# Kernel optimization log

Measured on AMD Instinct MI355X. Metric: run time of the kernel, lower is better.

Reference implementation:

```python
import jax, jax.numpy as jnp
import numpy as np

B, S, D, H = 2, 2048, 2048, 16
HD = D // H


def setup_inputs() -> dict:
    key = jax.random.key(0)
    kx, = jax.random.split(key, 1)
    return {
        "x": jax.random.normal(kx, (B, S, D), dtype=jnp.float32),
        "q_mask": jnp.ones((D, D), dtype=jnp.float32),
        "k_mask": jnp.ones((D, D), dtype=jnp.float32),
        "v_mask": jnp.ones((D, D), dtype=jnp.float32),
        "out_mask": jnp.ones((D, D), dtype=jnp.float32),
        "head_mask": jnp.ones((H,), dtype=jnp.float32),
        "attention_mask": jnp.ones((B, S), dtype=jnp.float32),
        "shared_weight": jnp.float32(1.0),
    }


def reference(x, q_mask, k_mask, v_mask, out_mask, head_mask, attention_mask, shared_weight):
    b, s, d = x.shape
    scale = jnp.float32(HD) ** -0.5

    def shared_linear(inp, mask):
        # F.linear(x, mask * shared_weight): out = inp @ (mask*sw).T
        return jnp.einsum("bsd,ed->bse", inp, mask * shared_weight)

    q = shared_linear(x, q_mask).reshape(b, s, H, HD).transpose(0, 2, 1, 3)  # [B,H,S,HD]
    k = shared_linear(x, k_mask).reshape(b, s, H, HD).transpose(0, 2, 1, 3)
    v = shared_linear(x, v_mask).reshape(b, s, H, HD).transpose(0, 2, 1, 3)

    hm = head_mask.reshape(1, H, 1, 1)
    q, k, v = q * hm, k * hm, v * hm

    scores = jnp.einsum("bhqd,bhkd->bhqk", q, k) * scale  # [B,H,S,S]

    # causal mask: upper triangle (j > i) -> -inf
    causal = jnp.triu(jnp.ones((s, s), dtype=bool), k=1)
    scores = jnp.where(causal, -jnp.inf, scores)

    # additive attention mask: (1 - m) * -10000, broadcast [B,1,1,S]
    scores = scores + (1.0 - attention_mask)[:, None, None, :] * -10000.0

    attn = jax.nn.softmax(scores, axis=-1)  # dropout is identity in eval / p=0

    out = jnp.einsum("bhqk,bhkd->bhqd", attn, v)          # [B,H,S,HD]
    out = out.transpose(0, 2, 1, 3).reshape(b, s, d)       # [B,S,D]
    return shared_linear(out, out_mask)
```

## Files before the change

kernel.cpp:

```cpp
#include <hip/hip_runtime.h>

#define B_  2
#define S_  2048
#define D_  2048
#define H_  16
#define HD_ 128

typedef __bf16 bf16;
typedef __bf16 bf16x4 __attribute__((ext_vector_type(4)));
typedef __bf16 bf16x8 __attribute__((ext_vector_type(8)));
typedef float  f32x4  __attribute__((ext_vector_type(4)));

__device__ __forceinline__ void gld_lds16(const void* g, void* l) {
    __builtin_amdgcn_global_load_lds(
        (const __attribute__((address_space(1))) unsigned int*)g,
        (__attribute__((address_space(3))) unsigned int*)l, 16, 0, 0);
}

__global__ __launch_bounds__(256)
void precast_kernel(const float* __restrict__ x, bf16* __restrict__ xh,
                    bf16* __restrict__ xl) {
    int i = (blockIdx.x * 256 + threadIdx.x) * 8;
    float4 a = *(const float4*)(x + i);
    float4 b = *(const float4*)(x + i + 4);
    float av[8] = {a.x, a.y, a.z, a.w, b.x, b.y, b.z, b.w};
    bf16x8 h8, l8;
#pragma unroll
    for (int e = 0; e < 8; e++) {
        bf16 hv = (bf16)av[e];
        h8[e] = hv;
        l8[e] = (bf16)(av[e] - (float)hv);
    }
    *(bf16x8*)(xh + i) = h8;
    *(bf16x8*)(xl + i) = l8;
}

__global__ __launch_bounds__(256)
void transpose_v(const bf16* __restrict__ vp, bf16* __restrict__ vt) {
    const int bh = blockIdx.x >> 5;
    const int s0 = (blockIdx.x & 31) * 64;
    const int t = threadIdx.x;
    __shared__ bf16 tile[128 * 72];
    const bf16* src = vp + (size_t)bh * S_ * HD_;
    bf16* dst = vt + (size_t)bh * HD_ * S_;

    {
        int r = t >> 2;
        int g = (t & 3) * 4;
#pragma unroll
        for (int w = 0; w < 4; w++) {
            bf16x8 v8 = *(const bf16x8*)&src[(size_t)(s0 + r) * HD_ + (g + w) * 8];
#pragma unroll
            for (int e = 0; e < 8; e++) tile[((g + w) * 8 + e) * 72 + r] = v8[e];
        }
    }
    __syncthreads();
    {
        int d = t >> 1;
        int sg0 = (t & 1) * 4;
#pragma unroll
        for (int w = 0; w < 4; w++) {
            int sg = sg0 + w;
            *(bf16x8*)&dst[(size_t)d * S_ + s0 + sg * 8] =
                *(const bf16x8*)&tile[d * 72 + sg * 8];
        }
    }
}

#define BK 64

template<int MODE>
__global__ __launch_bounds__(256, 3)
void gemm_nt(const bf16* __restrict__ Ah_g, const bf16* __restrict__ Al_g,
             const float* __restrict__ B0, const float* __restrict__ B1,
             const float* __restrict__ B2,
             const float* __restrict__ swp, const float* __restrict__ hm,
             bf16* __restrict__ qh_, bf16* __restrict__ ql_,
             bf16* __restrict__ kh_, bf16* __restrict__ kl_,
             bf16* __restrict__ vp_, float* __restrict__ Cf) {
    const int K = D_;
    __shared__ bf16 Ah[128 * 64];
    __shared__ bf16 Al[128 * 64];
    __shared__ bf16 Bs[128 * 64];
    const int t = threadIdx.x;
    const int wave = t >> 6, lane = t & 63;
    const int wr = wave >> 1, wc = wave & 1;
    const int m0 = blockIdx.y * 128, n0 = blockIdx.x * 128;
    const int lrow = lane & 15, lquad = lane >> 4;
    const float sw = swp[0];

    const int which = (MODE == 0) ? (n0 >> 11) : 0;
    const bool split = (MODE == 0) && (which < 2);

    const float* Bp;
    if (MODE == 0) {
        Bp = (which == 0) ? B0 : ((which == 1) ? B1 : B2);
        Bp += (size_t)(n0 & (D_ - 1)) * K;
    } else {
        Bp = B0 + (size_t)n0 * K;
    }

    const int srow8 = lane >> 3;
    const int sgrp  = lane & 7;
    const int g0 = (lquad)     ^ (lrow & 7);
    const int g1 = (lquad + 4) ^ (lrow & 7);

    f32x4 acc[4][4];
#pragma unroll
    for (int i = 0; i < 4; i++)
#pragma unroll
        for (int j = 0; j < 4; j++) acc[i][j] = (f32x4){0.f, 0.f, 0.f, 0.f};

    for (int k0 = 0; k0 < K; k0 += BK) {
#pragma unroll
        for (int p = 0; p < 4; p++) {
            int r = wave * 32 + p * 8 + srow8;
            int gcol = (sgrp ^ (r & 7)) * 8;
            gld_lds16(Ah_g + (size_t)(m0 + r) * K + k0 + gcol,
                      &Ah[(wave * 32 + p * 8) * 64]);
            if (split)
                gld_lds16(Al_g + (size_t)(m0 + r) * K + k0 + gcol,
                          &Al[(wave * 32 + p * 8) * 64]);
        }
#pragma unroll
        for (int p = 0; p < 4; p++) {
            int r = p * 32 + (t >> 3);
            int gcol = (sgrp ^ (r & 7)) * 8;
            const float* bp = Bp + (size_t)r * K + k0 + gcol;
            float4 blo = *(const float4*)bp;
            float4 bhi = *(const float4*)(bp + 4);
            bf16x8 b8;
            b8[0] = (bf16)(blo.x * sw); b8[1] = (bf16)(blo.y * sw);
            b8[2] = (bf16)(blo.z * sw); b8[3] = (bf16)(blo.w * sw);
            b8[4] = (bf16)(bhi.x * sw); b8[5] = (bf16)(bhi.y * sw);
            b8[6] = (bf16)(bhi.z * sw); b8[7] = (bf16)(bhi.w * sw);
            *(bf16x8*)&Bs[r * 64 + sgrp * 8] = b8;
        }
        __syncthreads();

#pragma unroll
        for (int kk = 0; kk < 2; kk++) {
            const int gA = kk ? g1 : g0;
            bf16x8 afh[4], afl[4], bfr[4];
#pragma unroll
            for (int i = 0; i < 4; i++) {
                int row = wr * 64 + i * 16 + lrow;
                afh[i] = *(const bf16x8*)&Ah[row * 64 + gA * 8];
                if (split) afl[i] = *(const bf16x8*)&Al[row * 64 + gA * 8];
            }
#pragma unroll
            for (int j = 0; j < 4; j++) {
                int row = wc * 64 + j * 16 + lrow;
                bfr[j] = *(const bf16x8*)&Bs[row * 64 + gA * 8];
            }
#pragma unroll
            for (int i = 0; i < 4; i++)
#pragma unroll
                for (int j = 0; j < 4; j++) {
                    acc[i][j] = __builtin_amdgcn_mfma_f32_16x16x32_bf16(
                        afh[i], bfr[j], acc[i][j], 0, 0, 0);
                    if (split)
                        acc[i][j] = __builtin_amdgcn_mfma_f32_16x16x32_bf16(
                            afl[i], bfr[j], acc[i][j], 0, 0, 0);
                }
        }
        __syncthreads();
    }

#pragma unroll
    for (int i = 0; i < 4; i++) {
#pragma unroll
        for (int j = 0; j < 4; j++) {
#pragma unroll
            for (int r = 0; r < 4; r++) {
                int m = m0 + wr * 64 + i * 16 + lquad * 4 + r;
                int n = n0 + wc * 64 + j * 16 + lrow;
                float v = acc[i][j][r];
                if (MODE == 0) {
                    int e = n & (D_ - 1);
                    int h = e >> 7, hd = e & (HD_ - 1);
                    int b = m >> 11, s = m & (S_ - 1);
                    v *= hm[h];
                    size_t idx = (((size_t)b * H_ + h) * S_ + s) * HD_ + hd;
                    if (which == 2) {
                        vp_[idx] = (bf16)v;
                    } else {
                        bf16 hv = (bf16)v;
                        bf16 lv = (bf16)(v - (float)hv);
                        if (which == 0) { qh_[idx] = hv; ql_[idx] = lv; }
                        else            { kh_[idx] = hv; kl_[idx] = lv; }
                    }
                } else {
                    Cf[(size_t)m * D_ + n] = v;
                }
            }
        }
    }
}

#define SPLD 72

__global__ __launch_bounds__(256, 2)
void attn_kernel(const bf16* __restrict__ qh_, const bf16* __restrict__ ql_,
                 const bf16* __restrict__ kh_, const bf16* __restrict__ kl_,
                 const bf16* __restrict__ vt_, const float* __restrict__ am,
                 bf16* __restrict__ outp) {
    const int bh = blockIdx.x & 31;
    const int qblk = 31 - (blockIdx.x >> 5);
    const int b = bh >> 4, h = bh & 15;
    const int i0 = qblk * 64;
    const int t = threadIdx.x, wave = t >> 6, lane = t & 63;
    const int lrow = lane & 15, quad = lane >> 4;

    __shared__ bf16 skh[64 * 128];
    __shared__ bf16 skl[64 * 128];
    __shared__ bf16 svt[128 * 64];
    __shared__ bf16 sp[4][16 * SPLD];

    const size_t kbase = (size_t)bh * S_ * HD_;
    const size_t vbase = (size_t)bh * HD_ * S_;

    const int qrow = i0 + wave * 16 + lrow;
    bf16x8 qhf[4], qlf[4];
#pragma unroll
    for (int c = 0; c < 4; c++) {
        qhf[c] = *(const bf16x8*)&qh_[kbase + (size_t)qrow * HD_ + c * 32 + quad * 8];
        qlf[c] = *(const bf16x8*)&ql_[kbase + (size_t)qrow * HD_ + c * 32 + quad * 8];
    }

    float m_i[4], l_i[4];
    f32x4 O[8];
#pragma unroll
    for (int r = 0; r < 4; r++) { m_i[r] = -INFINITY; l_i[r] = 0.f; }
#pragma unroll
    for (int n2 = 0; n2 < 8; n2++) O[n2] = (f32x4){0.f, 0.f, 0.f, 0.f};

    const float scale = 0.08838834764831845f;

    for (int j0 = 0; j0 <= i0; j0 += 64) {
        __syncthreads();
#pragma unroll
        for (int p = 0; p < 4; p++) {
            int rb = wave * 16 + p * 4;
            int r = rb + (lane >> 4);
            int gl = ((lane & 15) ^ (r & 7)) * 8;
            gld_lds16(kh_ + kbase + (size_t)(j0 + r) * HD_ + gl, &skh[rb * 128]);
            gld_lds16(kl_ + kbase + (size_t)(j0 + r) * HD_ + gl, &skl[rb * 128]);
        }
#pragma unroll
        for (int p = 0; p < 4; p++) {
            int db = wave * 32 + p * 8;
            int d = db + (lane >> 3);
            int gl = ((lane & 7) ^ (d & 7)) * 8;
            gld_lds16(vt_ + vbase + (size_t)d * S_ + j0 + gl, &svt[db * 64]);
        }
        __syncthreads();

        float amadd[4];
#pragma unroll
        for (int nt = 0; nt < 4; nt++)
            amadd[nt] = (1.0f - am[b * S_ + j0 + nt * 16 + lrow]) * -10000.0f;

        f32x4 s4[4];
#pragma unroll
        for (int nt = 0; nt < 4; nt++) s4[nt] = (f32x4){0.f, 0.f, 0.f, 0.f};
#pragma unroll
        for (int c = 0; c < 4; c++) {
#pragma unroll
            for (int nt = 0; nt < 4; nt++) {
                int ka = (nt * 16 + lrow) * 128 + (((c * 4 + quad) ^ (lrow & 7)) * 8);
                bf16x8 kb8 = *(const bf16x8*)&skh[ka];
                bf16x8 lb8 = *(const bf16x8*)&skl[ka];
                s4[nt] = __builtin_amdgcn_mfma_f32_16x16x32_bf16(qhf[c], kb8, s4[nt], 0, 0, 0);
                s4[nt] = __builtin_amdgcn_mfma_f32_16x16x32_bf16(qhf[c], lb8, s4[nt], 0, 0, 0);
                s4[nt] = __builtin_amdgcn_mfma_f32_16x16x32_bf16(qlf[c], kb8, s4[nt], 0, 0, 0);
            }
        }

        const bool diag = (j0 == i0);
#pragma unroll
        for (int r = 0; r < 4; r++) {
            const int rrow = wave * 16 + quad * 4 + r;
            float sv[4], pw[4];
            float mx = -INFINITY;
#pragma unroll
            for (int nt = 0; nt < 4; nt++) {
                float xv = s4[nt][r] * scale + amadd[nt];
                if (diag && (nt * 16 + lrow) > rrow) xv = -INFINITY;
                sv[nt] = xv;
                mx = fmaxf(mx, xv);
            }
#pragma unroll
            for (int off = 1; off < 16; off <<= 1) mx = fmaxf(mx, __shfl_xor(mx, off));
            float mnew = fmaxf(m_i[r], mx);
            float alpha = __expf(m_i[r] - mnew);
            float ps = 0.f;
#pragma unroll
            for (int nt = 0; nt < 4; nt++) { pw[nt] = __expf(sv[nt] - mnew); ps += pw[nt]; }
#pragma unroll
            for (int off = 1; off < 16; off <<= 1) ps += __shfl_xor(ps, off);
            l_i[r] = l_i[r] * alpha + ps;
            m_i[r] = mnew;
#pragma unroll
            for (int n2 = 0; n2 < 8; n2++) O[n2][r] *= alpha;
#pragma unroll
            for (int nt = 0; nt < 4; nt++)
                sp[wave][(quad * 4 + r) * SPLD + nt * 16 + lrow] = (bf16)pw[nt];
        }
        __asm__ volatile("s_waitcnt lgkmcnt(0)" ::: "memory");

#pragma unroll
        for (int k2 = 0; k2 < 2; k2++) {
            bf16x8 pf = *(const bf16x8*)&sp[wave][lrow * SPLD + k2 * 32 + quad * 8];
            const int gp = ((quad + k2 * 4) ^ (lrow & 7)) * 8;
#pragma unroll
            for (int n2 = 0; n2 < 8; n2++) {
                bf16x8 vf8 = *(const bf16x8*)&svt[(n2 * 16 + lrow) * 64 + gp];
                O[n2] = __builtin_amdgcn_mfma_f32_16x16x32_bf16(pf, vf8, O[n2], 0, 0, 0);
            }
        }
    }

    float inv[4];
#pragma unroll
    for (int r = 0; r < 4; r++) inv[r] = 1.0f / l_i[r];
#pragma unroll
    for (int n2 = 0; n2 < 8; n2++)
#pragma unroll
        for (int r = 0; r < 4; r++) {
            int srow = i0 + wave * 16 + quad * 4 + r;
            outp[((size_t)(b * S_ + srow)) * D_ + h * HD_ + n2 * 16 + lrow] =
                (bf16)(O[n2][r] * inv[r]);
        }
}

extern "C" void kernel_launch(void* const* d_in, const int* in_sizes, int n_in,
                              void* d_out, int out_size, void* d_ws, size_t ws_size,
                              hipStream_t stream) {
    const float* x  = (const float*)d_in[0];
    const float* qm = (const float*)d_in[1];
    const float* km = (const float*)d_in[2];
    const float* vm = (const float*)d_in[3];
    const float* om = (const float*)d_in[4];
    const float* hm = (const float*)d_in[5];
    const float* am = (const float*)d_in[6];
    const float* sw = (const float*)d_in[7];
    float* out = (float*)d_out;

    const size_t P = (size_t)B_ * H_ * S_ * HD_ * sizeof(bf16);
    char* ws = (char*)d_ws;
    bf16* xh = (bf16*)(ws + 0 * P);
    bf16* xl = (bf16*)(ws + 1 * P);
    bf16* qh = (bf16*)(ws + 2 * P);
    bf16* ql = (bf16*)(ws + 3 * P);
    bf16* kh = (bf16*)(ws + 4 * P);
    bf16* kl = (bf16*)(ws + 5 * P);
    bf16* vp = (bf16*)d_out;
    bf16* vt = (bf16*)((char*)d_out + P);
    bf16* attn_out = (bf16*)(ws + 0 * P);

    precast_kernel<<<(B_ * S_ * D_) / (256 * 8), 256, 0, stream>>>(x, xh, xl);

    gemm_nt<0><<<dim3(48, 32), 256, 0, stream>>>(
        xh, xl, qm, km, vm, sw, hm, qh, ql, kh, kl, vp, nullptr);

    transpose_v<<<1024, 256, 0, stream>>>(vp, vt);

    attn_kernel<<<1024, 256, 0, stream>>>(qh, ql, kh, kl, vt, am, attn_out);

    gemm_nt<1><<<dim3(16, 32), 256, 0, stream>>>(
        attn_out, nullptr, om, nullptr, nullptr, sw, hm,
        nullptr, nullptr, nullptr, nullptr, nullptr, out);
}
```

Baseline: 491.4 us.

## Replace projection GEMMs with double-buffered 512-thread pipelined bf16 GEMM and precast weights

Precasts the scaled fp32 weight masks to bf16 in separate kernels, so the GEMM loads both operands with direct global-to-LDS transfers instead of converting B in registers. A new templated 256x256/128x256 tile GEMM with 8 waves, double-buffered LDS, explicit vmcnt waits, barriers and setprio interleaves loads with MFMA work. The hi/lo split of x is folded into the K loop by running K twice (64 tiles) instead of issuing paired MFMAs. The V projection writes its transposed layout directly, which removes the separate transpose kernel. The cost is extra precast launches and workspace buffers, plus buffer aliasing inside d_out.

Measured after the change: 491.5 us. No clear change (+0.0%).

```diff
diff --git a/kernel.cpp b/kernel.cpp
--- a/kernel.cpp
+++ b/kernel.cpp
@@ -16,6 +16,14 @@
         (const __attribute__((address_space(1))) unsigned int*)g,
         (__attribute__((address_space(3))) unsigned int*)l, 16, 0, 0);
 }
+
+__device__ __forceinline__ f32x4 mfma16(bf16x8 a, bf16x8 b, f32x4 c) {
+    return __builtin_amdgcn_mfma_f32_16x16x32_bf16(a, b, c, 0, 0, 0);
+}
+
+#define BAR()        do { __builtin_amdgcn_s_barrier(); asm volatile("" ::: "memory"); } while (0)
+#define WAIT_LGKM0() do { asm volatile("s_waitcnt lgkmcnt(0)" ::: "memory"); \
+                          __builtin_amdgcn_sched_barrier(0); } while (0)
 
 __global__ __launch_bounds__(256)
 void precast_kernel(const float* __restrict__ x, bf16* __restrict__ xh,
@@ -36,163 +44,241 @@
 }
 
 __global__ __launch_bounds__(256)
-void transpose_v(const bf16* __restrict__ vp, bf16* __restrict__ vt) {
-    const int bh = blockIdx.x >> 5;
-    const int s0 = (blockIdx.x & 31) * 64;
-    const int t = threadIdx.x;
-    __shared__ bf16 tile[128 * 72];
-    const bf16* src = vp + (size_t)bh * S_ * HD_;
-    bf16* dst = vt + (size_t)bh * HD_ * S_;
-
-    {
-        int r = t >> 2;
-        int g = (t & 3) * 4;
-#pragma unroll
-        for (int w = 0; w < 4; w++) {
-            bf16x8 v8 = *(const bf16x8*)&src[(size_t)(s0 + r) * HD_ + (g + w) * 8];
-#pragma unroll
-            for (int e = 0; e < 8; e++) tile[((g + w) * 8 + e) * 72 + r] = v8[e];
-        }
-    }
-    __syncthreads();
-    {
-        int d = t >> 1;
-        int sg0 = (t & 1) * 4;
-#pragma unroll
-        for (int w = 0; w < 4; w++) {
-            int sg = sg0 + w;
-            *(bf16x8*)&dst[(size_t)d * S_ + s0 + sg * 8] =
-                *(const bf16x8*)&tile[d * 72 + sg * 8];
-        }
-    }
-}
-
-#define BK 64
-
-template<int MODE>
-__global__ __launch_bounds__(256, 3)
-void gemm_nt(const bf16* __restrict__ Ah_g, const bf16* __restrict__ Al_g,
-             const float* __restrict__ B0, const float* __restrict__ B1,
-             const float* __restrict__ B2,
-             const float* __restrict__ swp, const float* __restrict__ hm,
-             bf16* __restrict__ qh_, bf16* __restrict__ ql_,
-             bf16* __restrict__ kh_, bf16* __restrict__ kl_,
-             bf16* __restrict__ vp_, float* __restrict__ Cf) {
-    const int K = D_;
-    __shared__ bf16 Ah[128 * 64];
-    __shared__ bf16 Al[128 * 64];
-    __shared__ bf16 Bs[128 * 64];
+void precast_mask(const float* __restrict__ s0, bf16* __restrict__ d0,
+                  const float* __restrict__ s1, bf16* __restrict__ d1,
+                  const float* __restrict__ swp) {
+    const float sw = swp[0];
+    int bid = blockIdx.x;
+    const float* src = s0; bf16* dst = d0;
+    if (bid >= 2048) { src = s1; dst = d1; bid -= 2048; }
+    int i = (bid * 256 + threadIdx.x) * 8;
+    float4 a = *(const float4*)(src + i);
+    float4 b = *(const float4*)(src + i + 4);
+    bf16x8 o;
+    o[0] = (bf16)(a.x * sw); o[1] = (bf16)(a.y * sw);
+    o[2] = (bf16)(a.z * sw); o[3] = (bf16)(a.w * sw);
+    o[4] = (bf16)(b.x * sw); o[5] = (bf16)(b.y * sw);
+    o[6] = (bf16)(b.z * sw); o[7] = (bf16)(b.w * sw);
+    *(bf16x8*)(dst + i) = o;
+}
+
+template<int BM, int BN, int WM, int WN, int MODE>
+__global__ __launch_bounds__(512)
+void gemm8p(const bf16* __restrict__ Ah_g, const bf16* __restrict__ Al_g,
+            const bf16* __restrict__ Bq, const bf16* __restrict__ Bk,
+            const float* __restrict__ hm,
+            bf16* __restrict__ o_qh, bf16* __restrict__ o_ql,
+            bf16* __restrict__ o_kh, bf16* __restrict__ o_kl,
+            bf16* __restrict__ o_vt, float* __restrict__ o_f32,
+            int nt) {
+    constexpr int IM = BM / WM / 16;
+    constexpr int JN = BN / WN / 16;
+    constexpr int IH = IM / 2, JH = JN / 2;
+    constexpr int ISSA = BM / 64;
+    constexpr int ISSB = BN / 64;
+    constexpr int VMW = ISSA + ISSB;
+    constexpr int BUFE = (BM + BN) * 64;
+
+    __shared__ bf16 sm[2 * BUFE];
+
     const int t = threadIdx.x;
     const int wave = t >> 6, lane = t & 63;
-    const int wr = wave >> 1, wc = wave & 1;
-    const int m0 = blockIdx.y * 128, n0 = blockIdx.x * 128;
-    const int lrow = lane & 15, lquad = lane >> 4;
-    const float sw = swp[0];
-
-    const int which = (MODE == 0) ? (n0 >> 11) : 0;
-    const bool split = (MODE == 0) && (which < 2);
-
-    const float* Bp;
-    if (MODE == 0) {
-        Bp = (which == 0) ? B0 : ((which == 1) ? B1 : B2);
-        Bp += (size_t)(n0 & (D_ - 1)) * K;
-    } else {
-        Bp = B0 + (size_t)n0 * K;
-    }
-
-    const int srow8 = lane >> 3;
-    const int sgrp  = lane & 7;
-    const int g0 = (lquad)     ^ (lrow & 7);
-    const int g1 = (lquad + 4) ^ (lrow & 7);
-
-    f32x4 acc[4][4];
-#pragma unroll
-    for (int i = 0; i < 4; i++)
-#pragma unroll
-        for (int j = 0; j < 4; j++) acc[i][j] = (f32x4){0.f, 0.f, 0.f, 0.f};
-
-    for (int k0 = 0; k0 < K; k0 += BK) {
-#pragma unroll
-        for (int p = 0; p < 4; p++) {
-            int r = wave * 32 + p * 8 + srow8;
-            int gcol = (sgrp ^ (r & 7)) * 8;
-            gld_lds16(Ah_g + (size_t)(m0 + r) * K + k0 + gcol,
-                      &Ah[(wave * 32 + p * 8) * 64]);
-            if (split)
-                gld_lds16(Al_g + (size_t)(m0 + r) * K + k0 + gcol,
-                          &Al[(wave * 32 + p * 8) * 64]);
-        }
-#pragma unroll
-        for (int p = 0; p < 4; p++) {
-            int r = p * 32 + (t >> 3);
-            int gcol = (sgrp ^ (r & 7)) * 8;
-            const float* bp = Bp + (size_t)r * K + k0 + gcol;
-            float4 blo = *(const float4*)bp;
-            float4 bhi = *(const float4*)(bp + 4);
-            bf16x8 b8;
-            b8[0] = (bf16)(blo.x * sw); b8[1] = (bf16)(blo.y * sw);
-            b8[2] = (bf16)(blo.z * sw); b8[3] = (bf16)(blo.w * sw);
-            b8[4] = (bf16)(bhi.x * sw); b8[5] = (bf16)(bhi.y * sw);
-            b8[6] = (bf16)(bhi.z * sw); b8[7] = (bf16)(bhi.w * sw);
-            *(bf16x8*)&Bs[r * 64 + sgrp * 8] = b8;
-        }
+    const int lrow = lane & 15, quad = lane >> 4;
+    const int wr = wave / WN, wc = wave % WN;
+    const int m0 = blockIdx.y * BM, n0 = blockIdx.x * BN;
+
+    const int nsec = (MODE == 0) ? (n0 & (D_ - 1)) : n0;
+    const bf16* Bg = (MODE == 0 && n0 >= D_) ? Bk : Bq;
+
+    const int arow = wr * (BM / WM) + lrow;
+    const int brow = wc * (BN / WN) + lrow;
+    const int g0e = (quad ^ (lrow & 7)) * 8;
+    const int g1e = g0e ^ 32;
+
+    auto stage_A = [&](int kt, int p) {
+        const bf16* As = (MODE == 0 && kt >= 32) ? Al_g : Ah_g;
+        const int kc = ((MODE == 0) ? (kt & 31) : kt) * 64;
+        bf16* buf = sm + p * BUFE;
+        const int r0 = wave * (BM / 8);
+#pragma unroll
+        for (int pp = 0; pp < ISSA; pp++) {
+            int r = r0 + pp * 8 + (lane >> 3);
+            int gc = ((lane & 7) ^ (r & 7)) * 8;
+            gld_lds16(As + (size_t)(m0 + r) * D_ + kc + gc,
+                      buf + (r0 + pp * 8) * 64);
+        }
+    };
+    auto stage_B = [&](int kt, int p) {
+        const int kc = ((MODE == 0) ? (kt & 31) : kt) * 64;
+        bf16* buf = sm + p * BUFE + BM * 64;
+        const int r0 = wave * (BN / 8);
+#pragma unroll
+        for (int pp = 0; pp < ISSB; pp++) {
+            int r = r0 + pp * 8 + (lane >> 3);
+            int gc = ((lane & 7) ^ (r & 7)) * 8;
+            gld_lds16(Bg + (size_t)(nsec + r) * D_ + kc + gc,
+                      buf + (r0 + pp * 8) * 64);
+        }
+    };
+
+    f32x4 acc[IM][JN];
+#pragma unroll
+    for (int i = 0; i < IM; i++)
+#pragma unroll
+        for (int j = 0; j < JN; j++) acc[i][j] = (f32x4){0.f, 0.f, 0.f, 0.f};
+
+    stage_A(0, 0); stage_B(0, 0);
+    stage_A(1, 1); stage_B(1, 1);
+
+    const bf16 *Ab, *Bb;
+    auto rdA = [&](int ii, int ge) -> bf16x8 {
+        return *(const bf16x8*)&Ab[(arow + ii * 16) * 64 + ge];
+    };
+    auto rdB = [&](int jj, int ge) -> bf16x8 {
+        return *(const bf16x8*)&Bb[(brow + jj * 16) * 64 + ge];
+    };
+
+    int p = 0;
+    for (int kt = 0; kt < nt; ++kt) {
+        if (kt < nt - 1) {
+            if constexpr (VMW == 8) asm volatile("s_waitcnt vmcnt(8)" ::: "memory");
+            else                    asm volatile("s_waitcnt vmcnt(6)" ::: "memory");
+        } else {
+            asm volatile("s_waitcnt vmcnt(0)" ::: "memory");
+        }
+        BAR();
+        Ab = sm + p * BUFE;
+        Bb = Ab + BM * 64;
+
+        bf16x8 a[IH][2], b[JH][2], b2[JH][2];
+
+#pragma unroll
+        for (int i = 0; i < IH; i++) { a[i][0] = rdA(i, g0e); a[i][1] = rdA(i, g1e); }
+#pragma unroll
+        for (int j = 0; j < JH; j++) { b[j][0] = rdB(j, g0e); b[j][1] = rdB(j, g1e); }
+        BAR();
+        WAIT_LGKM0();
+        __builtin_amdgcn_s_setprio(1);
+#pragma unroll
+        for (int i = 0; i < IH; i++)
+#pragma unroll
+            for (int j = 0; j < JH; j++) {
+                acc[i][j] = mfma16(a[i][0], b[j][0], acc[i][j]);
+                acc[i][j] = mfma16(a[i][1], b[j][1], acc[i][j]);
+            }
+        __builtin_amdgcn_s_setprio(0);
+        BAR();
+
+#pragma unroll
+        for (int j = 0; j < JH; j++) { b2[j][0] = rdB(JH + j, g0e); b2[j][1] = rdB(JH + j, g1e); }
+        BAR();
+        WAIT_LGKM0();
+        __builtin_amdgcn_s_setprio(1);
+#pragma unroll
+        for (int i = 0; i < IH; i++)
+#pragma unroll
+            for (int j = 0; j < JH; j++) {
+                acc[i][JH + j] = mfma16(a[i][0], b2[j][0], acc[i][JH + j]);
+                acc[i][JH + j] = mfma16(a[i][1], b2[j][1], acc[i][JH + j]);
+            }
+        __builtin_amdgcn_s_setprio(0);
+        BAR();
+
+        if (kt + 2 < nt) stage_B(kt + 2, p);
+
+#pragma unroll
+        for (int i = 0; i < IH; i++) { a[i][0] = rdA(IH + i, g0e); a[i][1] = rdA(IH + i, g1e); }
+        BAR();
+        WAIT_LGKM0();
+        __builtin_amdgcn_s_setprio(1);
+#pragma unroll
+        for (int i = 0; i < IH; i++)
+#pragma unroll
+            for (int j = 0; j < JH; j++) {
+                acc[IH + i][j] = mfma16(a[i][0], b[j][0], acc[IH + i][j]);
+                acc[IH + i][j] = mfma16(a[i][1], b[j][1], acc[IH + i][j]);
+            }
+        __builtin_amdgcn_s_setprio(0);
+        BAR();
+
+        if (kt + 2 < nt) stage_A(kt + 2, p);
+
+        __builtin_amdgcn_s_setprio(1);
+#pragma unroll
+        for (int i = 0; i < IH; i++)
+#pragma unroll
+            for (int j = 0; j < JH; j++) {
+                acc[IH + i][JH + j] = mfma16(a[i][0], b2[j][0], acc[IH + i][JH + j]);
+                acc[IH + i][JH + j] = mfma16(a[i][1], b2[j][1], acc[IH + i][JH + j]);
+            }
+        __builtin_amdgcn_s_setprio(0);
+        p ^= 1;
+    }
+
+    if constexpr (MODE == 0) {
+        const bool isq = (n0 < D_);
+        bf16* oh = isq ? o_qh : o_kh;
+        bf16* ol = isq ? o_ql : o_kl;
+#pragma unroll
+        for (int j = 0; j < JN; j++) {
+            int nb = nsec + wc * (BN / WN) + j * 16;
+            int h = nb >> 7;
+            float hv = hm[h];
+#pragma unroll
+            for (int i = 0; i < IM; i++) {
+                int mB = m0 + wr * (BM / WM) + i * 16 + quad * 4;
+                int bb = mB >> 11, s = mB & (S_ - 1);
+                size_t idx0 = (((size_t)bb * H_ + h) * S_ + s) * HD_ + (nb & 127) + lrow;
+#pragma unroll
+                for (int r = 0; r < 4; r++) {
+                    float v = acc[i][j][r] * hv;
+                    bf16 hvv = (bf16)v;
+                    bf16 lvv = (bf16)(v - (float)hvv);
+                    oh[idx0 + (size_t)r * HD_] = hvv;
+                    ol[idx0 + (size_t)r * HD_] = lvv;
+                }
+            }
+        }
+    }
+    if constexpr (MODE == 1) {
         __syncthreads();
-
-#pragma unroll
-        for (int kk = 0; kk < 2; kk++) {
-            const int gA = kk ? g1 : g0;
-            bf16x8 afh[4], afl[4], bfr[4];
-#pragma unroll
-            for (int i = 0; i < 4; i++) {
-                int row = wr * 64 + i * 16 + lrow;
-                afh[i] = *(const bf16x8*)&Ah[row * 64 + gA * 8];
-                if (split) afl[i] = *(const bf16x8*)&Al[row * 64 + gA * 8];
-            }
-#pragma unroll
-            for (int j = 0; j < 4; j++) {
-                int row = wc * 64 + j * 16 + lrow;
-                bfr[j] = *(const bf16x8*)&Bs[row * 64 + gA * 8];
-            }
-#pragma unroll
-            for (int i = 0; i < 4; i++)
-#pragma unroll
-                for (int j = 0; j < 4; j++) {
-                    acc[i][j] = __builtin_amdgcn_mfma_f32_16x16x32_bf16(
-                        afh[i], bfr[j], acc[i][j], 0, 0, 0);
-                    if (split)
-                        acc[i][j] = __builtin_amdgcn_mfma_f32_16x16x32_bf16(
-                            afl[i], bfr[j], acc[i][j], 0, 0, 0);
-                }
+        bf16* tr = sm;
+#pragma unroll
+        for (int j = 0; j < JN; j++) {
+            int nl = wc * (BN / WN) + j * 16 + lrow;
+            float hv = hm[(n0 + nl) >> 7];
+#pragma unroll
+            for (int i = 0; i < IM; i++) {
+                int ml = wr * (BM / WM) + i * 16 + quad * 4;
+                bf16x4 pk;
+#pragma unroll
+                for (int r = 0; r < 4; r++) pk[r] = (bf16)(acc[i][j][r] * hv);
+                *(bf16x4*)&tr[nl * 136 + ml] = pk;
+            }
         }
         __syncthreads();
-    }
-
-#pragma unroll
-    for (int i = 0; i < 4; i++) {
-#pragma unroll
-        for (int j = 0; j < 4; j++) {
-#pragma unroll
-            for (int r = 0; r < 4; r++) {
-                int m = m0 + wr * 64 + i * 16 + lquad * 4 + r;
-                int n = n0 + wc * 64 + j * 16 + lrow;
-                float v = acc[i][j][r];
-                if (MODE == 0) {
-                    int e = n & (D_ - 1);
-                    int h = e >> 7, hd = e & (HD_ - 1);
-                    int b = m >> 11, s = m & (S_ - 1);
-                    v *= hm[h];
-                    size_t idx = (((size_t)b * H_ + h) * S_ + s) * HD_ + hd;
-                    if (which == 2) {
-                        vp_[idx] = (bf16)v;
-                    } else {
-                        bf16 hv = (bf16)v;
-                        bf16 lv = (bf16)(v - (float)hv);
-                        if (which == 0) { qh_[idx] = hv; ql_[idx] = lv; }
-                        else            { kh_[idx] = hv; kl_[idx] = lv; }
-                    }
-                } else {
-                    Cf[(size_t)m * D_ + n] = v;
-                }
+        const int bI = m0 >> 11;
+        const int s0 = m0 & (S_ - 1);
+#pragma unroll
+        for (int w = 0; w < 8; w++) {
+            int nrow = w * 32 + (t >> 4);
+            int c = t & 15;
+            bf16x8 vv = *(const bf16x8*)&tr[nrow * 136 + c * 8];
+            int ng = n0 + nrow;
+            int h = ng >> 7, hd = ng & 127;
+            *(bf16x8*)&o_vt[((size_t)(bI * H_ + h) * HD_ + hd) * S_ + s0 + c * 8] = vv;
+        }
+    }
+    if constexpr (MODE == 2) {
+#pragma unroll
+        for (int j = 0; j < JN; j++) {
+            int n = n0 + wc * (BN / WN) + j * 16 + lrow;
+#pragma unroll
+            for (int i = 0; i < IM; i++) {
+                int mB = m0 + wr * (BM / WM) + i * 16 + quad * 4;
+#pragma unroll
+                for (int r = 0; r < 4; r++)
+                    o_f32[(size_t)(mB + r) * D_ + n] = acc[i][j][r];
             }
         }
     }
@@ -355,20 +441,28 @@
     bf16* ql = (bf16*)(ws + 3 * P);
     bf16* kh = (bf16*)(ws + 4 * P);
     bf16* kl = (bf16*)(ws + 5 * P);
-    bf16* vp = (bf16*)d_out;
-    bf16* vt = (bf16*)((char*)d_out + P);
-    bf16* attn_out = (bf16*)(ws + 0 * P);
+    bf16* attn_out = xh;
+    bf16* vmb = xl;
+    bf16* omb = qh;
+    bf16* vt  = (bf16*)d_out;
+    bf16* qmb = (bf16*)((char*)d_out + 16u * 1024 * 1024);
+    bf16* kmb = (bf16*)((char*)d_out + 24u * 1024 * 1024);
 
     precast_kernel<<<(B_ * S_ * D_) / (256 * 8), 256, 0, stream>>>(x, xh, xl);
-
-    gemm_nt<0><<<dim3(48, 32), 256, 0, stream>>>(
-        xh, xl, qm, km, vm, sw, hm, qh, ql, kh, kl, vp, nullptr);
-
-    transpose_v<<<1024, 256, 0, stream>>>(vp, vt);
+    precast_mask<<<4096, 256, 0, stream>>>(qm, qmb, km, kmb, sw);
+
+    gemm8p<256, 256, 2, 4, 0><<<dim3(16, 16), 512, 0, stream>>>(
+        xh, xl, qmb, kmb, hm, qh, ql, kh, kl, nullptr, nullptr, 64);
+
+    precast_mask<<<2048, 256, 0, stream>>>(vm, vmb, nullptr, nullptr, sw);
+    gemm8p<128, 256, 2, 4, 1><<<dim3(8, 32), 512, 0, stream>>>(
+        xh, nullptr, vmb, nullptr, hm,
+        nullptr, nullptr, nullptr, nullptr, vt, nullptr, 32);
 
     attn_kernel<<<1024, 256, 0, stream>>>(qh, ql, kh, kl, vt, am, attn_out);
 
-    gemm_nt<1><<<dim3(16, 32), 256, 0, stream>>>(
-        attn_out, nullptr, om, nullptr, nullptr, sw, hm,
-        nullptr, nullptr, nullptr, nullptr, nullptr, out);
-}
+    precast_mask<<<2048, 256, 0, stream>>>(om, omb, nullptr, nullptr, sw);
+    gemm8p<256, 128, 4, 2, 2><<<dim3(16, 16), 512, 0, stream>>>(
+        attn_out, nullptr, omb, nullptr, hm,
+        nullptr, nullptr, nullptr, nullptr, nullptr, out, 32);
+}
```
